# Performance work log

Hardware: AMD Instinct MI355X
Metric: run time of the kernel (lower is better)

Reference implementation:

```python
import jax, jax.numpy as jnp
import numpy as np

B, Tin, Tout = 256, 32, 29
Venc, Vdec = 29, 72
E = 256; H = 256; L = 3; G = 4 * H; D = 2 * L  # bidirectional dirs * layers


def lstm_step(x, h, c, Wih0, Wih1, Whh, b):
    """One timestep of a 3-layer bidirectional LSTM (torch gate order i,f,g,o).
    x: [B, in], h/c: [D, B, H] in torch layout (layer-major, dir-minor)."""
    new_h, new_c = [], []
    inp = x
    for l in range(L):
        outs = []
        for d in range(2):
            idx = 2 * l + d
            Wih = Wih0[d] if l == 0 else Wih1[l - 1, d]
            g = inp @ Wih.T + h[idx] @ Whh[l, d].T + b[l, d]
            i_g, f_g, g_g, o_g = jnp.split(g, 4, axis=-1)
            cc = jax.nn.sigmoid(f_g) * c[idx] + jax.nn.sigmoid(i_g) * jnp.tanh(g_g)
            hh = jax.nn.sigmoid(o_g) * jnp.tanh(cc)
            new_h.append(hh); new_c.append(cc); outs.append(hh)
        inp = jnp.concatenate(outs, axis=-1)  # feeds next layer: [B, 2H]
    return jnp.stack(new_h), jnp.stack(new_c), inp


def proj(hid, W1, b1, W2, b2):
    """Linear over hidden dim then Linear over the layer*dir dim -- the exact
    math of torch's linear1 -> permute(2,1,0) -> linear2 -> permute(2,1,0)."""
    hn = jnp.einsum('lbh,gh->lbg', hid, W1) + b1            # [D, B, H]
    return jnp.einsum('lbh,ml->mbh', hn, W2) + b2[:, None, None]


def setup_inputs() -> dict:
    key = jax.random.key(0)
    ks = iter(jax.random.split(key, 64))
    def p(shape, scale=0.06):
        return jax.random.normal(next(ks), shape, jnp.float32) * scale
    return {
        "input": jax.random.randint(next(ks), (B, Tin), 0, Venc),
        "target": jax.random.randint(next(ks), (B, Tout), 0, Vdec),
        "teacher_force": 1,
        "enc_emb": p((Venc, E)), "dec_emb": p((Vdec, E)),
        "enc_Wih0": p((2, G, E)), "enc_Wih1": p((L - 1, 2, G, 2 * H)),
        "enc_Whh": p((L, 2, G, H)), "enc_b": p((L, 2, G)),
        "dec_Wih0": p((2, G, E)), "dec_Wih1": p((L - 1, 2, G, 2 * H)),
        "dec_Whh": p((L, 2, G, H)), "dec_b": p((L, 2, G)),
        "lin_h_W1": p((H, H)), "lin_h_b1": p((H,)), "lin_h_W2": p((D, D)), "lin_h_b2": p((D,)),
        "lin_c_W1": p((H, H)), "lin_c_b1": p((H,)), "lin_c_W2": p((D, D)), "lin_c_b2": p((D,)),
        "lin_a_W1": p((H, H)), "lin_a_b1": p((H,)), "lin_a_W2": p((D, D)), "lin_a_b2": p((D,)),
        "attn_W": p((E, E + H)), "attn_b": p((E,)),
        "fc_W": p((Vdec, 2 * H)), "fc_b": p((Vdec,)),
    }


def reference(input, target, teacher_force, enc_emb, dec_emb, enc_Wih0, enc_Wih1, enc_Whh, enc_b, dec_Wih0, dec_Wih1, dec_Whh, dec_b, lin_h_W1, lin_h_b1, lin_h_W2, lin_h_b2, lin_c_W1, lin_c_b1, lin_c_W2, lin_c_b2, lin_a_W1, lin_a_b1, lin_a_W2, lin_a_b2, attn_W, attn_b, fc_W, fc_b):
    Bb = input.shape[0]
    h0 = jnp.zeros((D, Bb, H), jnp.float32)

    # ---- encoder: step LSTM over Tin, projecting hidden per step for attention ----
    def enc_step(carry, x_t):
        h, c = carry
        h, c, _ = lstm_step(enc_emb[x_t], h, c, enc_Wih0, enc_Wih1, enc_Whh, enc_b)
        return (h, c), proj(h, lin_a_W1, lin_a_b1, lin_a_W2, lin_a_b2)

    (h, c), encoder_outputs = jax.lax.scan(enc_step, (h0, h0), input.T)  # [Tin, D, B, H]

    # ---- encoder->decoder state bridging (linear over H, linear over D) ----
    dec_h = proj(h, lin_h_W1, lin_h_b1, lin_h_W2, lin_h_b2)
    dec_c = proj(c, lin_c_W1, lin_c_b1, lin_c_W2, lin_c_b2)

    def dec_core(h, c, tok):
        emb = dec_emb[tok]                                # [B, E]
        energies = h[None] * encoder_outputs              # [Tin, D, B, H]
        aw = jax.nn.softmax(energies, axis=0)             # attn over source time
        ctx = (aw * encoder_outputs).sum(0).mean(0)       # [B, H]
        x = jnp.concatenate([emb, ctx], -1) @ attn_W.T + attn_b
        h, c, top = lstm_step(x, h, c, dec_Wih0, dec_Wih1, dec_Whh, dec_b)
        return h, c, top @ fc_W.T + fc_b, aw.sum(-1)      # logits [B,V], aw [Tin,D,B]

    if teacher_force:
        def step(carry, tok):
            h, c = carry
            h, c, logits, _ = dec_core(h, c, tok)
            return (h, c), logits
        _, logits_seq = jax.lax.scan(step, (dec_h, dec_c), target[:, :Tout - 1].T)
        attn_seq = jnp.zeros((Tout - 1, Tin, D, Bb), jnp.float32)
    else:
        def step(carry, _):
            h, c, tok = carry
            h, c, logits, aw = dec_core(h, c, tok)
            nxt = jnp.argmax(jax.nn.softmax(logits, -1), -1).astype(tok.dtype)
            return (h, c, nxt), (logits, aw)
        tok0 = jnp.ones((Bb,), input.dtype)
        _, (logits_seq, attn_seq) = jax.lax.scan(step, (dec_h, dec_c, tok0), None, length=Tout - 1)

    pred0 = jnp.zeros((1, Bb, Vdec), jnp.float32).at[0, :, 1].set(1.0)
    predicted = jnp.concatenate([pred0, logits_seq], 0)   # [Tout, B, Vdec]
    attn_weights = jnp.concatenate([jnp.zeros((1, Tin, D, Bb), jnp.float32), attn_seq], 0)
    return predicted, attn_weights
```

## Files before the change

### kernel.cpp

```cpp
#include <hip/hip_runtime.h>
#include <math.h>

#define BB 256
#define TIN 32
#define TOUT 29
#define VDEC 72
#define EDIM 256
#define HDIM 256
#define DD 6
#define BH (BB*HDIM)
#define NBLK 256

typedef unsigned short u16;
typedef unsigned int u32;
typedef __bf16 bf16x8 __attribute__((ext_vector_type(8)));
typedef float f32x4 __attribute__((ext_vector_type(4)));
typedef u16 u16x8 __attribute__((ext_vector_type(8)));

__device__ __forceinline__ float sigmf(float x){ return 1.0f/(1.0f+__expf(-x)); }
__device__ __forceinline__ float tanhf_fast(float x){ return 1.0f - 2.0f/(1.0f+__expf(2.0f*x)); }
__device__ __forceinline__ u16 f2bf(float f){
  u32 u = __builtin_bit_cast(u32, f);
  u32 r = (u + 0x7fffu + ((u>>16)&1u)) >> 16;
  return (u16)r;
}
__device__ __forceinline__ float bf2f(u16 s){
  u32 u = ((u32)s)<<16; return __builtin_bit_cast(float, u);
}
__device__ __forceinline__ bf16x8 ldbf8(const u16* p){
  u16x8 t = *(const u16x8*)p; return __builtin_bit_cast(bf16x8, t);
}
__device__ __forceinline__ bf16x8 ldbf8v(const u16* p){
  u16x8 t = *(const volatile u16x8*)p; return __builtin_bit_cast(bf16x8, t);
}
__device__ __forceinline__ float ldbfv(const u16* p){ return bf2f(*(const volatile u16*)p); }
__device__ __forceinline__ float ldfv(const float* p){ return *(const volatile float*)p; }
__device__ __forceinline__ f32x4 mfma16(bf16x8 a, bf16x8 b, f32x4 c){
  return __builtin_amdgcn_mfma_f32_16x16x32_bf16(a, b, c, 0, 0, 0);
}

struct GmS { float As[32][33]; float Ws[256][34]; };
union SharedU {
  struct { float Gt[2][4][32][18]; } st;
  GmS gm2[2];
  struct { float s[512]; float p4[VDEC][4]; float lg[VDEC]; float ctxp[2][256]; int tok; } fc;
};

__device__ __forceinline__ void gridbar(u32* arr, u32* gen, u32 g, int bid, bool fast){
  __syncthreads();
  if (fast){
    if (threadIdx.x == 0)
      __hip_atomic_store(&arr[bid], g, __ATOMIC_RELAXED, __HIP_MEMORY_SCOPE_AGENT);
    if (bid == 0){
      if (threadIdx.x < 256)
        while (__hip_atomic_load(&arr[threadIdx.x], __ATOMIC_RELAXED, __HIP_MEMORY_SCOPE_AGENT) < g)
          __builtin_amdgcn_s_sleep(1);
      __syncthreads();
      if (threadIdx.x == 0)
        __hip_atomic_store(gen, g, __ATOMIC_RELAXED, __HIP_MEMORY_SCOPE_AGENT);
    } else if (threadIdx.x == 0){
      while (__hip_atomic_load(gen, __ATOMIC_RELAXED, __HIP_MEMORY_SCOPE_AGENT) < g)
        __builtin_amdgcn_s_sleep(1);
    }
  } else {
    if (threadIdx.x == 0)
      __hip_atomic_store(&arr[bid], g, __ATOMIC_RELEASE, __HIP_MEMORY_SCOPE_AGENT);
    if (bid == 0){
      if (threadIdx.x < 256)
        while (__hip_atomic_load(&arr[threadIdx.x], __ATOMIC_RELAXED, __HIP_MEMORY_SCOPE_AGENT) < g)
          __builtin_amdgcn_s_sleep(1);
      __syncthreads();
      if (threadIdx.x == 0)
        __hip_atomic_store(gen, g, __ATOMIC_RELEASE, __HIP_MEMORY_SCOPE_AGENT);
    } else if (threadIdx.x == 0){
      while (__hip_atomic_load(gen, __ATOMIC_RELAXED, __HIP_MEMORY_SCOPE_AGENT) < g)
        __builtin_amdgcn_s_sleep(1);
    }
    __builtin_amdgcn_fence(__ATOMIC_ACQUIRE, "agent");
  }
  __syncthreads();
}

__global__ void fill_zero_u32(u32* __restrict__ p, int n){
  int i = blockIdx.x*256 + threadIdx.x;
  if (i < n) p[i] = 0u;
}

__global__ void init_out_kernel(float* __restrict__ out, int n){
  int i = blockIdx.x*256 + threadIdx.x;
  if (i >= n) return;
  float v = 0.0f;
  if (i < BB*VDEC && (i % VDEC) == 1) v = 1.0f;
  out[i] = v;
}

__global__ void bias2d_kernel(const float* __restrict__ W2a, const float* __restrict__ b1a, const float* __restrict__ b2a,
                              const float* __restrict__ W2h, const float* __restrict__ b1h, const float* __restrict__ b2h,
                              const float* __restrict__ W2c, const float* __restrict__ b1c, const float* __restrict__ b2c,
                              float* __restrict__ outp){
  int g = threadIdx.x;
  const float* W2[3] = {W2a, W2h, W2c};
  const float* b1[3] = {b1a, b1h, b1c};
  const float* b2[3] = {b2a, b2h, b2c};
  for (int p = 0; p < 3; p++)
    for (int m = 0; m < 6; m++){
      float s = 0.f;
      for (int l = 0; l < 6; l++) s += W2[p][m*6+l];
      outp[p*1536 + m*256 + g] = s * b1[p][g] + b2[p][m];
    }
}

__global__ void embed_enc_kernel(const int* __restrict__ input, const float* __restrict__ enc_emb,
                                 u16* __restrict__ x_emb){
  int i = blockIdx.x*256 + threadIdx.x;
  int e = i & 255, b = (i >> 8) & 255, t = i >> 16;
  x_emb[i] = f2bf(enc_emb[(size_t)input[b*TIN + t]*EDIM + e]);
}

__global__ void pack_w_kernel(const float* __restrict__ Wih, const float* __restrict__ Whh,
                              u16* __restrict__ dst, int K1, int K){
  int k = blockIdx.x*256 + threadIdx.x;
  int row = blockIdx.y;
  int d = row >> 10, rr = row & 1023;
  int ht = rr >> 6, r = rr & 63;
  int g = (r>>4)*256 + ht*16 + (r&15);
  float v;
  if (k < K1) v = Wih[((size_t)d*1024 + g)*K1 + k];
  else        v = Whh[((size_t)d*1024 + g)*256 + (k - K1)];
  dst[(size_t)row*K + k] = f2bf(v);
}

__global__ void pack_wfused_kernel(const float* __restrict__ Wih0, const float* __restrict__ attn_W,
                                   const float* __restrict__ Whh, u16* __restrict__ dst){
  int k = blockIdx.x*256 + threadIdx.x;
  int row = blockIdx.y;
  int d = row >> 10, rr = row & 1023;
  int ht = rr >> 6, r = rr & 63;
  int g = (r>>4)*256 + ht*16 + (r&15);
  float v;
  if (k >= 512) v = Whh[((size_t)d*1024 + g)*256 + (k - 512)];
  else {
    const float* wr = Wih0 + ((size_t)d*1024 + g)*256;
    float s = 0.f;
    #pragma unroll 4
    for (int o = 0; o < 256; o++) s += wr[o] * attn_W[(size_t)o*512 + k];
    v = s;
  }
  dst[(size_t)row*768 + k] = f2bf(v);
}

__global__ void biasfold_kernel(const float* __restrict__ Wih0, const float* __restrict__ attn_b,
                                const float* __restrict__ dec_b, float* __restrict__ outb){
  int i = blockIdx.x*256 + threadIdx.x;
  int d = i >> 10, g = i & 1023;
  const float* wr = Wih0 + ((size_t)d*1024 + g)*256;
  float s = dec_b[d*1024 + g];
  #pragma unroll 4
  for (int o = 0; o < 256; o++) s += wr[o]*attn_b[o];
  outb[i] = s;
}

template<int K1>
__device__ __forceinline__ void stage_phase(SharedU* shp, int mt, int y,
    const u16* __restrict__ inp, const u16* __restrict__ Wpk, const float* __restrict__ bias_l,
    const u16* __restrict__ hR, u16* __restrict__ hW, float* __restrict__ cBuf,
    u16* __restrict__ inp_out, float* __restrict__ h_all_t, int l){
  auto& ss = shp->st;
  constexpr int K = K1 + 256;
  constexpr int HK = K/2;
  int tid = threadIdx.x;
  int m_base = mt*32;
  int d = y >> 4, ht = y & 15;
  int idx = 2*l + d;
  int q8 = tid >> 6, lane = tid & 63;
  int qg = q8 & 3, kh2 = q8 >> 2;
  int r = lane & 15, lq = lane >> 4;
  const u16* a0p = inp + (size_t)(m_base + r)*K1 + lq*8;
  const u16* a1p = a0p + (size_t)16*K1;
  const u16* h0p = hR + (size_t)idx*BH + (size_t)(m_base + r)*HDIM + lq*8;
  const u16* h1p = h0p + 16*HDIM;
  const u16* wp  = Wpk + (size_t)((d*16+ht)*64 + qg*16 + r)*K + lq*8;
  const int cbase = kh2*HK;
  f32x4 acc0 = {0.f,0.f,0.f,0.f}, acc1 = {0.f,0.f,0.f,0.f};
  #pragma unroll
  for (int c = 0; c < HK; c += 32){
    int col = cbase + c;
    bool ina = (col < K1);
    const u16* pa0 = ina ? (a0p + col) : (h0p + (col - K1));
    const u16* pa1 = ina ? (a1p + col) : (h1p + (col - K1));
    bf16x8 a0 = ldbf8v(pa0);
    bf16x8 a1 = ldbf8v(pa1);
    bf16x8 bq = ldbf8(wp + col);
    acc0 = mfma16(a0, bq, acc0);
    acc1 = mfma16(a1, bq, acc1);
  }
  #pragma unroll
  for (int rr = 0; rr < 4; rr++){
    ss.Gt[kh2][qg][lq*4 + rr][r]      = acc0[rr];
    ss.Gt[kh2][qg][16 + lq*4 + rr][r] = acc1[rr];
  }
  __syncthreads();
  const float* bias = bias_l + d*1024;
  {
    int bb = tid >> 4, h2 = tid & 15;
    int b = m_base + bb, h = ht*16 + h2;
    float iv = ss.Gt[0][0][bb][h2] + ss.Gt[1][0][bb][h2] + bias[h];
    float fv = ss.Gt[0][1][bb][h2] + ss.Gt[1][1][bb][h2] + bias[256 + h];
    float gv = ss.Gt[0][2][bb][h2] + ss.Gt[1][2][bb][h2] + bias[512 + h];
    float ov = ss.Gt[0][3][bb][h2] + ss.Gt[1][3][bb][h2] + bias[768 + h];
    size_t off = (size_t)idx*BH + (size_t)b*HDIM + h;
    float cold = cBuf[off];
    float cc = sigmf(fv)*cold + sigmf(iv)*tanhf_fast(gv);
    float hv = sigmf(ov)*tanhf_fast(cc);
    cBuf[off] = cc;
    u16 hb = f2bf(hv);
    hW[off] = hb;
    inp_out[(size_t)b*512 + d*HDIM + h] = hb;
    if (h_all_t) h_all_t[off] = hv;
  }
}

__device__ __forceinline__ void mix_one(int b, int h, const float* __restrict__ inp,
    float* __restrict__ outp, const float* __restrict__ W2, int t){
  size_t base2 = ((size_t)t*6)*BH + (size_t)b*256 + h;
  float v[6];
  #pragma unroll
  for (int l = 0; l < 6; l++) v[l] = ldfv(&inp[base2 + (size_t)l*BH]);
  #pragma unroll
  for (int m = 0; m < 6; m++){
    float s = 0.f;
    #pragma unroll
    for (int l = 0; l < 6; l++) s += W2[m*6+l]*v[l];
    outp[base2 + (size_t)m*BH] = s;
  }
}

__device__ __forceinline__ void gemm_tile(GmS& sg, int tid, int m_base,
    const float* __restrict__ A, float* __restrict__ C, const float* __restrict__ W,
    const float* __restrict__ bias2d, u16* __restrict__ Cbf){
  int rg = tid >> 5, cg = tid & 31;
  float acc[4][8];
  #pragma unroll
  for (int i=0;i<4;i++)
    #pragma unroll
    for (int j=0;j<8;j++) acc[i][j]=0.f;
  for (int k0 = 0; k0 < 256; k0 += 32){
    #pragma unroll
    for (int p=0;p<4;p++) sg.As[rg + p*8][cg] = ldfv(&A[(size_t)(m_base + rg + p*8)*256 + k0 + cg]);
    #pragma unroll
    for (int p=0;p<32;p++) sg.Ws[rg + p*8][cg] = W[(size_t)(rg + p*8)*256 + k0 + cg];
    __syncthreads();
    #pragma unroll
    for (int kk=0; kk<32; kk++){
      float a[4], w[8];
      #pragma unroll
      for (int i=0;i<4;i++) a[i] = sg.As[rg*4+i][kk];
      #pragma unroll
      for (int j=0;j<8;j++) w[j] = sg.Ws[cg + 32*j][kk];
      #pragma unroll
      for (int i=0;i<4;i++)
        #pragma unroll
        for (int j=0;j<8;j++) acc[i][j] += a[i]*w[j];
    }
    __syncthreads();
  }
  #pragma unroll
  for (int i=0;i<4;i++){
    int row = m_base + rg*4 + i;
    int bm = (row >> 8) % 6;
    #pragma unroll
    for (int j=0;j<8;j++){
      int col = cg + 32*j;
      float v = acc[i][j] + bias2d[bm*256 + col];
      if (C)   C[(size_t)row*256 + col] = v;
      if (Cbf) Cbf[(size_t)row*256 + col] = f2bf(v);
    }
  }
}

__device__ __forceinline__ void attn_phase(SharedU* shp, int b, int step,
    const u16* __restrict__ hR, const u16* __restrict__ eo, u16* __restrict__ cat,
    const int* __restrict__ tf, float* __restrict__ attn_out,
    const int* __restrict__ target, float* __restrict__ outp,
    const float* __restrict__ dec_emb, const u16* __restrict__ top,
    const float* __restrict__ fc_W, const float* __restrict__ fc_b){
  auto& sf = shp->fc;
  int tid = threadIdx.x;
  if (step > 0){
    sf.s[tid] = ldbfv(&top[(size_t)b*512 + tid]);
    __syncthreads();
    if (tid < 4*VDEC){
      int v = tid >> 2, part = tid & 3;
      int k0 = part*128;
      const float* wr = fc_W + (size_t)v*512;
      float a = 0.f;
      #pragma unroll 4
      for (int k = k0; k < k0+128; k++) a += sf.s[k]*wr[k];
      sf.p4[v][part] = a;
    }
    __syncthreads();
    if (tid < VDEC){
      float a = fc_b[tid] + sf.p4[tid][0] + sf.p4[tid][1] + sf.p4[tid][2] + sf.p4[tid][3];
      outp[((size_t)step*BB + b)*VDEC + tid] = a;
      sf.lg[tid] = a;
    }
    __syncthreads();
  }
  int tok;
  if (tf[0]) tok = target[b*TOUT + step];
  else if (step == 0) tok = 1;
  else {
    if (tid == 0){
      int bi = 0; float bv = sf.lg[0];
      for (int v = 1; v < VDEC; v++){ float x = sf.lg[v]; if (x > bv){ bv = x; bi = v; } }
      sf.tok = bi;
    }
    __syncthreads();
    tok = sf.tok;
  }
  if (tid < 256) cat[(size_t)b*512 + tid] = f2bf(dec_emb[(size_t)tok*EDIM + tid]);
  int hc = tid & 255, dhalf = tid >> 8;
  bool wa = (tf[0] == 0);
  float acc = 0.f;
  for (int dd = 0; dd < 3; dd++){
    int d = dhalf*3 + dd;
    float hv = ldbfv(&hR[(size_t)d*BH + (size_t)b*256 + hc]);
    const u16* ep = eo + (size_t)d*BH + (size_t)b*256 + hc;
    float se = 0.f, ac = 0.f;
    #pragma unroll 8
    for (int t = 0; t < TIN; t++){
      float ev = bf2f(ep[(size_t)t*(DD*BH)]);
      float e = __expf(hv*ev);
      se += e; ac += e*ev;
    }
    acc += ac/se;
    if (wa){
      float inv = 1.f/se;
      for (int t = 0; t < TIN; t++){
        float ev = bf2f(ep[(size_t)t*(DD*BH)]);
        atomicAdd(&attn_out[(((size_t)(step+1)*TIN + t)*DD + d)*BB + b], __expf(hv*ev)*inv);
      }
    }
  }
  sf.ctxp[dhalf][hc] = acc;
  __syncthreads();
  if (tid < 256)
    cat[(size_t)b*512 + 256 + tid] = f2bf((sf.ctxp[0][tid] + sf.ctxp[1][tid])*(1.0f/6.0f));
}

__device__ __forceinline__ void fc_final_phase(SharedU* shp, int b,
    const u16* __restrict__ top, const float* __restrict__ fc_W,
    const float* __restrict__ fc_b, float* __restrict__ outp){
  auto& sf = shp->fc;
  int tid = threadIdx.x;
  sf.s[tid] = ldbfv(&top[(size_t)b*512 + tid]);
  __syncthreads();
  if (tid < 4*VDEC){
    int v = tid >> 2, part = tid & 3;
    int k0 = part*128;
    const float* wr = fc_W + (size_t)v*512;
    float a = 0.f;
    #pragma unroll 4
    for (int k = k0; k < k0+128; k++) a += sf.s[k]*wr[k];
    sf.p4[v][part] = a;
  }
  __syncthreads();
  if (tid < VDEC){
    float a = fc_b[tid] + sf.p4[tid][0] + sf.p4[tid][1] + sf.p4[tid][2] + sf.p4[tid][3];
    outp[((size_t)(TOUT-1)*BB + b)*VDEC + tid] = a;
  }
}

__global__ __launch_bounds__(512, 2) void mega_kernel(
    const int* __restrict__ target, const int* __restrict__ tf,
    const float* __restrict__ dec_emb, const u16* __restrict__ x_emb,
    const u16* __restrict__ wp_e0, const u16* __restrict__ wp_e1, const u16* __restrict__ wp_e2,
    const u16* __restrict__ wp_d0f, const u16* __restrict__ wp_d1, const u16* __restrict__ wp_d2,
    const float* __restrict__ enc_b, const float* __restrict__ dec_b, const float* __restrict__ fb0,
    const float* __restrict__ lin_h_W1, const float* __restrict__ lin_c_W1, const float* __restrict__ lin_a_W1,
    const float* __restrict__ lin_h_W2, const float* __restrict__ lin_c_W2, const float* __restrict__ lin_a_W2,
    const float* __restrict__ bias2d,
    const float* __restrict__ fc_W, const float* __restrict__ fc_b,
    float* __restrict__ out,
    float* __restrict__ h_all, float* __restrict__ tmp6, float* __restrict__ tmp6c,
    float* __restrict__ dec_c, u16* __restrict__ enc_hA, float* __restrict__ enc_c,
    u16* __restrict__ enc_hB, u16* __restrict__ dec_hA, u16* __restrict__ dec_hB,
    u16* __restrict__ bufA, u16* __restrict__ bufB, u16* __restrict__ cat,
    u16* __restrict__ eo_bf, u32* __restrict__ barblk)
{
  __shared__ SharedU sh;
  __shared__ u32 ord_sh;
  const int bid = blockIdx.x, tid = threadIdx.x;
  u32* arr = barblk;
  u32* gen = barblk + 320;
  u32* ctr = barblk + 336;
  u32* badflag = barblk + 352;
  u32 g = 0;

  u32 xcc;
  asm volatile("s_getreg_b32 %0, hwreg(HW_REG_XCC_ID)" : "=s"(xcc));
  xcc &= 7u;
  if (tid == 0){
    u32 o = __hip_atomic_fetch_add(&ctr[xcc], 1u, __ATOMIC_RELAXED, __HIP_MEMORY_SCOPE_AGENT);
    ord_sh = o;
    if (o >= 32u)
      __hip_atomic_store(badflag, 1u, __ATOMIC_RELAXED, __HIP_MEMORY_SCOPE_AGENT);
  }
  gridbar(arr, gen, ++g, bid, false);
  bool fast = (__hip_atomic_load(badflag, __ATOMIC_RELAXED, __HIP_MEMORY_SCOPE_AGENT) == 0u);
  int mt, y;
  if (fast){ mt = (int)xcc; y = (int)ord_sh; }
  else     { mt = bid & 7;  y = bid >> 3;    }
  const int half = tid >> 8, htid = tid & 255;

  for (int t = 0; t < TIN; t++){
    const u16* hRb = (t & 1) ? enc_hB : enc_hA;
    u16*       hWb = (t & 1) ? enc_hA : enc_hB;
    float* hat = h_all + (size_t)t*DD*BH;
    stage_phase<256>(&sh, mt, y, x_emb + (size_t)t*BB*EDIM, wp_e0, enc_b,        hRb, hWb, enc_c, bufA, hat, 0);
    gridbar(arr, gen, ++g, bid, fast);
    stage_phase<512>(&sh, mt, y, bufA,                      wp_e1, enc_b + 2048, hRb, hWb, enc_c, bufB, hat, 1);
    gridbar(arr, gen, ++g, bid, fast);
    stage_phase<512>(&sh, mt, y, bufB,                      wp_e2, enc_b + 4096, hRb, hWb, enc_c, bufA, hat, 2);
    gridbar(arr, gen, ++g, bid, fast);
  }

  {
    int b = mt*32 + y;
    if (half == 0) mix_one(b, htid, h_all + (size_t)31*DD*BH, tmp6,  lin_h_W2, 0);
    else           mix_one(b, htid, enc_c,                    tmp6c, lin_c_W2, 0);
    __syncthreads();
    for (int t2 = half*16; t2 < half*16 + 16; t2++)
      mix_one(b, htid, h_all, h_all, lin_a_W2, t2);
  }
  gridbar(arr, gen, ++g, bid, fast);
  if (y < 6)       gemm_tile(sh.gm2[half], htid, (y*8 + mt)*32,     tmp6,  nullptr, lin_h_W1, bias2d + 1536, dec_hA);
  else if (y < 12) gemm_tile(sh.gm2[half], htid, ((y-6)*8 + mt)*32, tmp6c, dec_c,   lin_c_W1, bias2d + 3072, nullptr);
  #pragma unroll
  for (int jj = 0; jj < 3; jj++){
    int j = half*3 + jj;
    gemm_tile(sh.gm2[half], htid, ((y + 32*j)*8 + mt)*32, h_all, nullptr, lin_a_W1, bias2d, eo_bf);
  }
  gridbar(arr, gen, ++g, bid, fast);

  float* attn_out = out + (size_t)TOUT*BB*VDEC;
  int b = mt*32 + y;
  for (int i = 0; i < TOUT-1; i++){
    const u16* hRb = (i & 1) ? dec_hB : dec_hA;
    u16*       hWb = (i & 1) ? dec_hA : dec_hB;
    attn_phase(&sh, b, i, hRb, eo_bf, cat, tf, attn_out, target, out, dec_emb, bufA, fc_W, fc_b);
    gridbar(arr, gen, ++g, bid, fast);
    stage_phase<512>(&sh, mt, y, cat,  wp_d0f, fb0,          hRb, hWb, dec_c, bufA, nullptr, 0);
    gridbar(arr, gen, ++g, bid, fast);
    stage_phase<512>(&sh, mt, y, bufA, wp_d1,  dec_b + 2048, hRb, hWb, dec_c, bufB, nullptr, 1);
    gridbar(arr, gen, ++g, bid, fast);
    stage_phase<512>(&sh, mt, y, bufB, wp_d2,  dec_b + 4096, hRb, hWb, dec_c, bufA, nullptr, 2);
    gridbar(arr, gen, ++g, bid, fast);
  }
  fc_final_phase(&sh, b, bufA, fc_W, fc_b, out);
}


extern "C" void kernel_launch(void* const* d_in, const int* in_sizes, int n_in,
                              void* d_out, int out_size, void* d_ws, size_t ws_size,
                              hipStream_t stream){
  (void)in_sizes; (void)n_in; (void)out_size; (void)ws_size;
  const int*   input    = (const int*)d_in[0];
  const int*   target   = (const int*)d_in[1];
  const int*   tf       = (const int*)d_in[2];
  const float* enc_emb  = (const float*)d_in[3];
  const float* dec_emb  = (const float*)d_in[4];
  const float* enc_Wih0 = (const float*)d_in[5];
  const float* enc_Wih1 = (const float*)d_in[6];
  const float* enc_Whh  = (const float*)d_in[7];
  const float* enc_b    = (const float*)d_in[8];
  const float* dec_Wih0 = (const float*)d_in[9];
  const float* dec_Wih1 = (const float*)d_in[10];
  const float* dec_Whh  = (const float*)d_in[11];
  const float* dec_b    = (const float*)d_in[12];
  const float* lin_h_W1 = (const float*)d_in[13];
  const float* lin_h_b1 = (const float*)d_in[14];
  const float* lin_h_W2 = (const float*)d_in[15];
  const float* lin_h_b2 = (const float*)d_in[16];
  const float* lin_c_W1 = (const float*)d_in[17];
  const float* lin_c_b1 = (const float*)d_in[18];
  const float* lin_c_W2 = (const float*)d_in[19];
  const float* lin_c_b2 = (const float*)d_in[20];
  const float* lin_a_W1 = (const float*)d_in[21];
  const float* lin_a_b1 = (const float*)d_in[22];
  const float* lin_a_W2 = (const float*)d_in[23];
  const float* lin_a_b2 = (const float*)d_in[24];
  const float* attn_W   = (const float*)d_in[25];
  const float* attn_b   = (const float*)d_in[26];
  const float* fc_W     = (const float*)d_in[27];
  const float* fc_b     = (const float*)d_in[28];
  float* out = (float*)d_out;

  char* base = (char*)d_ws;
  size_t off = 0;
  auto alloc = [&](size_t bytes)->char*{
    char* p = base + off; off += (bytes + 255) & ~(size_t)255; return p;
  };
  float* h_all  = (float*)alloc(sizeof(float)*(size_t)TIN*DD*BH);
  float* tmp6   = (float*)alloc(sizeof(float)*(size_t)DD*BH);
  float* tmp6c  = (float*)alloc(sizeof(float)*(size_t)DD*BH);
  float* dec_c  = (float*)alloc(sizeof(float)*(size_t)DD*BH);
  float* bias2d = (float*)alloc(sizeof(float)*3*6*256);
  u16*   enc_hA = (u16*)alloc(sizeof(u16)*(size_t)DD*BH + sizeof(float)*(size_t)DD*BH);
  float* enc_c  = (float*)(enc_hA + (size_t)DD*BH);
  u16* enc_hB = (u16*)alloc(sizeof(u16)*(size_t)DD*BH);
  u16* dec_hA = (u16*)alloc(sizeof(u16)*(size_t)DD*BH);
  u16* dec_hB = (u16*)alloc(sizeof(u16)*(size_t)DD*BH);
  u16* x_emb  = (u16*)alloc(sizeof(u16)*(size_t)TIN*BB*EDIM);
  u16* bufA   = (u16*)alloc(sizeof(u16)*(size_t)BB*512);
  u16* bufB   = (u16*)alloc(sizeof(u16)*(size_t)BB*512);
  u16* cat    = (u16*)alloc(sizeof(u16)*(size_t)BB*512);
  u16* eo_bf  = (u16*)alloc(sizeof(u16)*(size_t)TIN*DD*BH);
  u16* wp_e0  = (u16*)alloc(sizeof(u16)*(size_t)2048*512);
  u16* wp_e1  = (u16*)alloc(sizeof(u16)*(size_t)2048*768);
  u16* wp_e2  = (u16*)alloc(sizeof(u16)*(size_t)2048*768);
  u16* wp_d0f = (u16*)alloc(sizeof(u16)*(size_t)2048*768);
  u16* wp_d1  = (u16*)alloc(sizeof(u16)*(size_t)2048*768);
  u16* wp_d2  = (u16*)alloc(sizeof(u16)*(size_t)2048*768);
  float* fb0  = (float*)alloc(sizeof(float)*2048);
  u32* barblk = (u32*)alloc(sizeof(u32)*512);

  const int outn = TOUT*BB*VDEC + TOUT*TIN*DD*BB;
  init_out_kernel<<<(outn+255)/256, 256, 0, stream>>>(out, outn);
  fill_zero_u32<<<(DD*BH*6/4 + 255)/256, 256, 0, stream>>>((u32*)enc_hA, DD*BH*6/4);
  fill_zero_u32<<<2, 256, 0, stream>>>(barblk, 512);
  bias2d_kernel<<<1, 256, 0, stream>>>(lin_a_W2, lin_a_b1, lin_a_b2,
                                       lin_h_W2, lin_h_b1, lin_h_b2,
                                       lin_c_W2, lin_c_b1, lin_c_b2, bias2d);
  embed_enc_kernel<<<(TIN*BB*EDIM)/256, 256, 0, stream>>>(input, enc_emb, x_emb);
  pack_w_kernel<<<dim3(2,2048), 256, 0, stream>>>(enc_Wih0, enc_Whh,                       wp_e0, 256, 512);
  pack_w_kernel<<<dim3(3,2048), 256, 0, stream>>>(enc_Wih1, enc_Whh + 2*1024*256,          wp_e1, 512, 768);
  pack_w_kernel<<<dim3(3,2048), 256, 0, stream>>>(enc_Wih1 + (size_t)2*1024*512, enc_Whh + 4*1024*256, wp_e2, 512, 768);
  pack_wfused_kernel<<<dim3(3,2048), 256, 0, stream>>>(dec_Wih0, attn_W, dec_Whh,          wp_d0f);
  biasfold_kernel<<<8, 256, 0, stream>>>(dec_Wih0, attn_b, dec_b, fb0);
  pack_w_kernel<<<dim3(3,2048), 256, 0, stream>>>(dec_Wih1, dec_Whh + 2*1024*256,          wp_d1, 512, 768);
  pack_w_kernel<<<dim3(3,2048), 256, 0, stream>>>(dec_Wih1 + (size_t)2*1024*512, dec_Whh + 4*1024*256, wp_d2, 512, 768);

  mega_kernel<<<NBLK, 512, 0, stream>>>(
      target, tf, dec_emb, x_emb,
      wp_e0, wp_e1, wp_e2, wp_d0f, wp_d1, wp_d2,
      enc_b, dec_b, fb0,
      lin_h_W1, lin_c_W1, lin_a_W1, lin_h_W2, lin_c_W2, lin_a_W2,
      bias2d, fc_W, fc_b, out,
      h_all, tmp6, tmp6c, dec_c, enc_hA, enc_c, enc_hB, dec_hA, dec_hB,
      bufA, bufB, cat, eo_bf, barblk);
}
```

Baseline: 3.909 ms.

## Replace grid-wide barriers with per-XCD group barriers and drop redundant stage output

The global 256-block barrier is replaced, on the fast path, by per-XCC counter barriers that only sync the 32 blocks sharing a batch tile (mt), relying on the fact that each batch slice's data stays within its XCC group. The post-encoder GEMM tiles are reassigned so each group only produces its own batch rows, and the last encoder layer no longer writes the unused layer output. This removes cross-die barrier latency on every timestep, at the cost of correctness depending on the data partition being strictly local to each group.

```diff
diff --git a/kernel.cpp b/kernel.cpp
--- a/kernel.cpp
+++ b/kernel.cpp
@@ -46,39 +46,41 @@
   struct { float s[512]; float p4[VDEC][4]; float lg[VDEC]; float ctxp[2][256]; int tok; } fc;
 };
 
-__device__ __forceinline__ void gridbar(u32* arr, u32* gen, u32 g, int bid, bool fast){
+__device__ __forceinline__ void xbar(u32* barblk, int mt, u32 g, int bid, bool fast){
   __syncthreads();
   if (fast){
-    if (threadIdx.x == 0)
-      __hip_atomic_store(&arr[bid], g, __ATOMIC_RELAXED, __HIP_MEMORY_SCOPE_AGENT);
-    if (bid == 0){
-      if (threadIdx.x < 256)
-        while (__hip_atomic_load(&arr[threadIdx.x], __ATOMIC_RELAXED, __HIP_MEMORY_SCOPE_AGENT) < g)
-          __builtin_amdgcn_s_sleep(1);
-      __syncthreads();
-      if (threadIdx.x == 0)
-        __hip_atomic_store(gen, g, __ATOMIC_RELAXED, __HIP_MEMORY_SCOPE_AGENT);
-    } else if (threadIdx.x == 0){
-      while (__hip_atomic_load(gen, __ATOMIC_RELAXED, __HIP_MEMORY_SCOPE_AGENT) < g)
-        __builtin_amdgcn_s_sleep(1);
-    }
+    u32* cnt  = barblk + 384 + mt*32;
+    u32* genx = cnt + 16;
+    if (threadIdx.x == 0){
+      u32 old = __hip_atomic_fetch_add(cnt, 1u, __ATOMIC_RELAXED, __HIP_MEMORY_SCOPE_AGENT);
+      if (old == 31u){
+        __hip_atomic_store(cnt, 0u, __ATOMIC_RELAXED, __HIP_MEMORY_SCOPE_AGENT);
+        __hip_atomic_store(genx, g, __ATOMIC_RELEASE, __HIP_MEMORY_SCOPE_AGENT);
+      } else {
+        while (__hip_atomic_load(genx, __ATOMIC_RELAXED, __HIP_MEMORY_SCOPE_AGENT) < g)
+          __builtin_amdgcn_s_sleep(2);
+      }
+    }
+    __syncthreads();
   } else {
+    u32* arr = barblk;
+    u32* gen = barblk + 320;
     if (threadIdx.x == 0)
       __hip_atomic_store(&arr[bid], g, __ATOMIC_RELEASE, __HIP_MEMORY_SCOPE_AGENT);
     if (bid == 0){
       if (threadIdx.x < 256)
         while (__hip_atomic_load(&arr[threadIdx.x], __ATOMIC_RELAXED, __HIP_MEMORY_SCOPE_AGENT) < g)
-          __builtin_amdgcn_s_sleep(1);
+          __builtin_amdgcn_s_sleep(2);
       __syncthreads();
       if (threadIdx.x == 0)
         __hip_atomic_store(gen, g, __ATOMIC_RELEASE, __HIP_MEMORY_SCOPE_AGENT);
     } else if (threadIdx.x == 0){
       while (__hip_atomic_load(gen, __ATOMIC_RELAXED, __HIP_MEMORY_SCOPE_AGENT) < g)
-        __builtin_amdgcn_s_sleep(1);
+        __builtin_amdgcn_s_sleep(2);
     }
     __builtin_amdgcn_fence(__ATOMIC_ACQUIRE, "agent");
-  }
-  __syncthreads();
+    __syncthreads();
+  }
 }
 
 __global__ void fill_zero_u32(u32* __restrict__ p, int n){
@@ -194,6 +196,7 @@
     acc0 = mfma16(a0, bq, acc0);
     acc1 = mfma16(a1, bq, acc1);
   }
+  __syncthreads();
   #pragma unroll
   for (int rr = 0; rr < 4; rr++){
     ss.Gt[kh2][qg][lq*4 + rr][r]      = acc0[rr];
@@ -215,7 +218,7 @@
     cBuf[off] = cc;
     u16 hb = f2bf(hv);
     hW[off] = hb;
-    inp_out[(size_t)b*512 + d*HDIM + h] = hb;
+    if (inp_out) inp_out[(size_t)b*512 + d*HDIM + h] = hb;
     if (h_all_t) h_all_t[off] = hv;
   }
 }
@@ -391,8 +394,6 @@
   __shared__ SharedU sh;
   __shared__ u32 ord_sh;
   const int bid = blockIdx.x, tid = threadIdx.x;
-  u32* arr = barblk;
-  u32* gen = barblk + 320;
   u32* ctr = barblk + 336;
   u32* badflag = barblk + 352;
   u32 g = 0;
@@ -406,56 +407,57 @@
     if (o >= 32u)
       __hip_atomic_store(badflag, 1u, __ATOMIC_RELAXED, __HIP_MEMORY_SCOPE_AGENT);
   }
-  gridbar(arr, gen, ++g, bid, false);
+  xbar(barblk, 0, ++g, bid, false);
   bool fast = (__hip_atomic_load(badflag, __ATOMIC_RELAXED, __HIP_MEMORY_SCOPE_AGENT) == 0u);
   int mt, y;
   if (fast){ mt = (int)xcc; y = (int)ord_sh; }
   else     { mt = bid & 7;  y = bid >> 3;    }
   const int half = tid >> 8, htid = tid & 255;
+  const int b = mt*32 + y;
 
   for (int t = 0; t < TIN; t++){
     const u16* hRb = (t & 1) ? enc_hB : enc_hA;
     u16*       hWb = (t & 1) ? enc_hA : enc_hB;
     float* hat = h_all + (size_t)t*DD*BH;
     stage_phase<256>(&sh, mt, y, x_emb + (size_t)t*BB*EDIM, wp_e0, enc_b,        hRb, hWb, enc_c, bufA, hat, 0);
-    gridbar(arr, gen, ++g, bid, fast);
+    xbar(barblk, mt, ++g, bid, fast);
     stage_phase<512>(&sh, mt, y, bufA,                      wp_e1, enc_b + 2048, hRb, hWb, enc_c, bufB, hat, 1);
-    gridbar(arr, gen, ++g, bid, fast);
-    stage_phase<512>(&sh, mt, y, bufB,                      wp_e2, enc_b + 4096, hRb, hWb, enc_c, bufA, hat, 2);
-    gridbar(arr, gen, ++g, bid, fast);
-  }
+    xbar(barblk, mt, ++g, bid, fast);
+    stage_phase<512>(&sh, mt, y, bufB,                      wp_e2, enc_b + 4096, hRb, hWb, enc_c, nullptr, hat, 2);
+  }
+  xbar(barblk, mt, ++g, bid, fast);
 
   {
-    int b = mt*32 + y;
     if (half == 0) mix_one(b, htid, h_all + (size_t)31*DD*BH, tmp6,  lin_h_W2, 0);
     else           mix_one(b, htid, enc_c,                    tmp6c, lin_c_W2, 0);
     __syncthreads();
     for (int t2 = half*16; t2 < half*16 + 16; t2++)
       mix_one(b, htid, h_all, h_all, lin_a_W2, t2);
   }
-  gridbar(arr, gen, ++g, bid, fast);
-  if (y < 6)       gemm_tile(sh.gm2[half], htid, (y*8 + mt)*32,     tmp6,  nullptr, lin_h_W1, bias2d + 1536, dec_hA);
-  else if (y < 12) gemm_tile(sh.gm2[half], htid, ((y-6)*8 + mt)*32, tmp6c, dec_c,   lin_c_W1, bias2d + 3072, nullptr);
+  xbar(barblk, mt, ++g, bid, fast);
+  if (y < 6){
+    if (half == 0) gemm_tile(sh.gm2[0], htid, y*256 + mt*32, tmp6,  nullptr, lin_h_W1, bias2d + 1536, dec_hA);
+    else           gemm_tile(sh.gm2[1], htid, y*256 + mt*32, tmp6c, dec_c,   lin_c_W1, bias2d + 3072, nullptr);
+  }
   #pragma unroll
   for (int jj = 0; jj < 3; jj++){
-    int j = half*3 + jj;
-    gemm_tile(sh.gm2[half], htid, ((y + 32*j)*8 + mt)*32, h_all, nullptr, lin_a_W1, bias2d, eo_bf);
-  }
-  gridbar(arr, gen, ++g, bid, fast);
+    int k2 = y*6 + half*3 + jj;
+    gemm_tile(sh.gm2[half], htid, k2*256 + mt*32, h_all, nullptr, lin_a_W1, bias2d, eo_bf);
+  }
+  xbar(barblk, mt, ++g, bid, fast);
 
   float* attn_out = out + (size_t)TOUT*BB*VDEC;
-  int b = mt*32 + y;
   for (int i = 0; i < TOUT-1; i++){
     const u16* hRb = (i & 1) ? dec_hB : dec_hA;
     u16*       hWb = (i & 1) ? dec_hA : dec_hB;
     attn_phase(&sh, b, i, hRb, eo_bf, cat, tf, attn_out, target, out, dec_emb, bufA, fc_W, fc_b);
-    gridbar(arr, gen, ++g, bid, fast);
+    xbar(barblk, mt, ++g, bid, fast);
     stage_phase<512>(&sh, mt, y, cat,  wp_d0f, fb0,          hRb, hWb, dec_c, bufA, nullptr, 0);
-    gridbar(arr, gen, ++g, bid, fast);
+    xbar(barblk, mt, ++g, bid, fast);
     stage_phase<512>(&sh, mt, y, bufA, wp_d1,  dec_b + 2048, hRb, hWb, dec_c, bufB, nullptr, 1);
-    gridbar(arr, gen, ++g, bid, fast);
+    xbar(barblk, mt, ++g, bid, fast);
     stage_phase<512>(&sh, mt, y, bufB, wp_d2,  dec_b + 4096, hRb, hWb, dec_c, bufA, nullptr, 2);
-    gridbar(arr, gen, ++g, bid, fast);
+    xbar(barblk, mt, ++g, bid, fast);
   }
   fc_final_phase(&sh, b, bufA, fc_W, fc_b, out);
 }
@@ -523,12 +525,12 @@
   u16* wp_d1  = (u16*)alloc(sizeof(u16)*(size_t)2048*768);
   u16* wp_d2  = (u16*)alloc(sizeof(u16)*(size_t)2048*768);
   float* fb0  = (float*)alloc(sizeof(float)*2048);
-  u32* barblk = (u32*)alloc(sizeof(u32)*512);
+  u32* barblk = (u32*)alloc(sizeof(u32)*1024);
 
   const int outn = TOUT*BB*VDEC + TOUT*TIN*DD*BB;
   init_out_kernel<<<(outn+255)/256, 256, 0, stream>>>(out, outn);
   fill_zero_u32<<<(DD*BH*6/4 + 255)/256, 256, 0, stream>>>((u32*)enc_hA, DD*BH*6/4);
-  fill_zero_u32<<<2, 256, 0, stream>>>(barblk, 512);
+  fill_zero_u32<<<4, 256, 0, stream>>>(barblk, 1024);
   bias2d_kernel<<<1, 256, 0, stream>>>(lin_a_W2, lin_a_b1, lin_a_b2,
                                        lin_h_W2, lin_h_b1, lin_h_b2,
                                        lin_c_W2, lin_c_b1, lin_c_b2, bias2d);
```

Result: no change. 3.896 ms (-0.3%).
